# Optimization experiments

Hardware: AMD Instinct MI355X
Metric: run time of the kernel (lower is better)

The kernel has to match this reference:

```python
import jax, jax.numpy as jnp
import numpy as np

# Segment boundaries from the original hard-coded slices: 13,13,13,9,4 repeated twice
SEG_BOUNDS = [0, 13, 26, 39, 48, 52, 65, 78, 91, 100, 104]


def segmented_log_softmax(x):
    # x: [B, 104]; independent log-softmax over each of the 10 fixed segments
    return jnp.concatenate(
        [jax.nn.log_softmax(x[:, a:b], axis=-1)
         for a, b in zip(SEG_BOUNDS[:-1], SEG_BOUNDS[1:])], axis=-1)


def setup_inputs() -> dict:
    key = jax.random.key(0)
    ks = jax.random.split(key, 8)
    B, H, D = 8192, 2048, 104
    return {
        "line": jax.random.normal(ks[0], (B, D), dtype=jnp.float32),
        "hidden": jax.random.normal(ks[1], (B, H), dtype=jnp.float32),
        "U_w": jax.random.normal(ks[2], (H, H), dtype=jnp.float32) * 0.02,
        "U_b": jax.random.normal(ks[3], (H,), dtype=jnp.float32) * 0.02,
        "W_w": jax.random.normal(ks[4], (H, D), dtype=jnp.float32) * 0.02,
        "W_b": jax.random.normal(ks[5], (H,), dtype=jnp.float32) * 0.02,
        "V_w": jax.random.normal(ks[6], (D, H), dtype=jnp.float32) * 0.02,
        "V_b": jax.random.normal(ks[7], (D,), dtype=jnp.float32) * 0.02,
    }


def reference(line, hidden, U_w, U_b, W_w, W_b, V_w, V_b):
    # h_t = sigmoid(U(hidden) + W(line)); torch Linear: y = x @ W.T + b
    h_t = jax.nn.sigmoid(hidden @ U_w.T + U_b + line @ W_w.T + W_b)  # [B, H]
    pred = h_t @ V_w.T + V_b                                          # [B, 104]
    pred_logsoft = segmented_log_softmax(pred)                        # [B, 104]
    return pred_logsoft, h_t
```

## Files before the change

kernel.cpp:

```cpp
#include <hip/hip_runtime.h>
#include <cstdint>
#include <cstddef>


typedef __bf16 bf16x8 __attribute__((ext_vector_type(8)));
typedef float  f32x4  __attribute__((ext_vector_type(4)));
typedef unsigned short ushort8 __attribute__((ext_vector_type(8)));
typedef float  float4v __attribute__((ext_vector_type(4)));

#define BB 8192
#define HH 2048
#define DD 104

static __device__ __forceinline__ unsigned short f2bf(float f) {
  unsigned u = __float_as_uint(f);
  unsigned r = (u + 0x7FFFu + ((u >> 16) & 1u)) >> 16;
  return (unsigned short)r;
}

#define GLD_LDS(g, l)                                                          \
  __builtin_amdgcn_global_load_lds(                                            \
      (__attribute__((address_space(1))) void*)(g),                            \
      (__attribute__((address_space(3))) void*)(l), 16, 0, 0)

#define MEMFENCE asm volatile("" ::: "memory")
#define MFMA16(a, b, c) __builtin_amdgcn_mfma_f32_16x16x32_bf16((a), (b), (c), 0, 0, 0)

__global__ __launch_bounds__(256) void conv_bf16_kernel(
    const float* __restrict__ hidden, const float* __restrict__ Uw,
    unsigned short* __restrict__ out_hidden, unsigned short* __restrict__ out_U) {
  long long i = ((long long)blockIdx.x * blockDim.x + threadIdx.x) * 8;
  const float* src; unsigned short* dst; long long off;
  if (i < (long long)BB * HH) { src = hidden; dst = out_hidden; off = i; }
  else { src = Uw; dst = out_U; off = i - (long long)BB * HH; }
  float4v a = *(const float4v*)(src + off);
  float4v b = *(const float4v*)(src + off + 4);
  ushort8 o;
  o[0]=f2bf(a[0]); o[1]=f2bf(a[1]); o[2]=f2bf(a[2]); o[3]=f2bf(a[3]);
  o[4]=f2bf(b[0]); o[5]=f2bf(b[1]); o[6]=f2bf(b[2]); o[7]=f2bf(b[3]);
  *(ushort8*)(dst + off) = o;
}

__global__ __launch_bounds__(256) void pad_bf16_kernel(
    const float* __restrict__ line, const float* __restrict__ Ww,
    const float* __restrict__ Vw,
    unsigned short* __restrict__ line_pad, unsigned short* __restrict__ Ww_pad,
    unsigned short* __restrict__ Vw_pad) {
  int i = blockIdx.x * blockDim.x + threadIdx.x;
  const int N1 = BB * 128;
  const int N2 = N1 + HH * 128;
  if (i < N1) {
    int r = i >> 7, c = i & 127;
    line_pad[i] = (c < DD) ? f2bf(line[r * DD + c]) : (unsigned short)0;
  } else if (i < N2) {
    int j = i - N1; int r = j >> 7, c = j & 127;
    Ww_pad[j] = (c < DD) ? f2bf(Ww[r * DD + c]) : (unsigned short)0;
  } else {
    int j = i - N2; int r = j >> 11, c = j & 2047;
    Vw_pad[j] = (r < DD) ? f2bf(Vw[r * 2048 + c]) : (unsigned short)0;
  }
}

template <int BUF, bool STAGE, bool TAIL>
static __device__ __forceinline__ void ktile(
    int kb_n,
    unsigned short* smem,
    const unsigned short* pAh, const unsigned short* pAl,
    const unsigned short* pBu, const unsigned short* pBw,
    unsigned short* dA, unsigned short* dB,
    int aoffs, int boffs, f32x4 (&acc)[8][4]) {
  constexpr int SB = BUF ^ 1;
  const unsigned short* Ab = smem + BUF * 16384;
  const unsigned short* Bb = smem + 32768 + BUF * 16384;
  const bool hi = STAGE && (kb_n >= 2048);
  const unsigned short* sA0 = hi ? pAl + (kb_n - 2048) : pAh + kb_n;
  const unsigned short* sB0 = hi ? pBw + (kb_n - 2048) : pBu + kb_n;
  const int rstr = hi ? 128 : 2048;
  bf16x8 a[8], b0, b1;

#pragma unroll
  for (int mi = 0; mi < 8; ++mi) a[mi] = *(const bf16x8*)(Ab + aoffs + mi * 512);
  b0 = *(const bf16x8*)(Bb + boffs);
  b1 = *(const bf16x8*)(Bb + boffs + 512);
  if (STAGE) {
    GLD_LDS(sA0, dA + SB * 16384);
    GLD_LDS(sA0 + 128 * rstr, dA + SB * 16384 + 4096);
  }
  __builtin_amdgcn_s_setprio(1);
#pragma unroll
  for (int mi = 0; mi < 8; ++mi) {
    acc[mi][0] = MFMA16(a[mi], b0, acc[mi][0]);
    acc[mi][1] = MFMA16(a[mi], b1, acc[mi][1]);
  }
  __builtin_amdgcn_s_setprio(0);
  MEMFENCE; __builtin_amdgcn_s_barrier(); MEMFENCE;

  b0 = *(const bf16x8*)(Bb + boffs + 1024);
  b1 = *(const bf16x8*)(Bb + boffs + 1536);
  if (STAGE) {
    GLD_LDS(sB0, dB + SB * 16384);
    GLD_LDS(sB0 + 128 * rstr, dB + SB * 16384 + 4096);
  }
  __builtin_amdgcn_s_setprio(1);
#pragma unroll
  for (int mi = 0; mi < 8; ++mi) {
    acc[mi][2] = MFMA16(a[mi], b0, acc[mi][2]);
    acc[mi][3] = MFMA16(a[mi], b1, acc[mi][3]);
  }
  __builtin_amdgcn_s_setprio(0);
  if (TAIL) { asm volatile("s_waitcnt vmcnt(0)" ::: "memory"); }
  else      { asm volatile("s_waitcnt vmcnt(4)" ::: "memory"); }
  MEMFENCE; __builtin_amdgcn_s_barrier(); MEMFENCE;

#pragma unroll
  for (int mi = 0; mi < 8; ++mi) a[mi] = *(const bf16x8*)(Ab + 8192 + aoffs + mi * 512);
  b0 = *(const bf16x8*)(Bb + 8192 + boffs);
  b1 = *(const bf16x8*)(Bb + 8192 + boffs + 512);
  if (STAGE) {
    GLD_LDS(sA0 + 32, dA + SB * 16384 + 8192);
    GLD_LDS(sA0 + 32 + 128 * rstr, dA + SB * 16384 + 8192 + 4096);
  }
  __builtin_amdgcn_s_setprio(1);
#pragma unroll
  for (int mi = 0; mi < 8; ++mi) {
    acc[mi][0] = MFMA16(a[mi], b0, acc[mi][0]);
    acc[mi][1] = MFMA16(a[mi], b1, acc[mi][1]);
  }
  __builtin_amdgcn_s_setprio(0);
  MEMFENCE; __builtin_amdgcn_s_barrier(); MEMFENCE;

  b0 = *(const bf16x8*)(Bb + 8192 + boffs + 1024);
  b1 = *(const bf16x8*)(Bb + 8192 + boffs + 1536);
  if (STAGE) {
    GLD_LDS(sB0 + 32, dB + SB * 16384 + 8192);
    GLD_LDS(sB0 + 32 + 128 * rstr, dB + SB * 16384 + 8192 + 4096);
  }
  __builtin_amdgcn_s_setprio(1);
#pragma unroll
  for (int mi = 0; mi < 8; ++mi) {
    acc[mi][2] = MFMA16(a[mi], b0, acc[mi][2]);
    acc[mi][3] = MFMA16(a[mi], b1, acc[mi][3]);
  }
  __builtin_amdgcn_s_setprio(0);
  if (!TAIL) { asm volatile("s_waitcnt vmcnt(4)" ::: "memory"); }
  MEMFENCE; __builtin_amdgcn_s_barrier(); MEMFENCE;
}

__global__ __launch_bounds__(512, 2) void gemm1_kernel(
    const unsigned short* __restrict__ Ahid,
    const unsigned short* __restrict__ Aline,
    const unsigned short* __restrict__ BU,
    const unsigned short* __restrict__ BW,
    const float* __restrict__ Ub, const float* __restrict__ Wb,
    float* __restrict__ outH, unsigned short* __restrict__ outHbf) {
  __shared__ unsigned short smem[65536];
  const int t = threadIdx.x;
  const int l = t & 63;
  const int wid = t >> 6;
  const int wr = wid >> 2, wc = wid & 3;

  const int bid = blockIdx.x;
  const int wg = (bid & 7) * 32 + (bid >> 3);
  const int brow = (wg >> 3) * 256;
  const int bcol = (wg & 7) * 256;

  const int frow = l & 15, lhi = l >> 4;
  const int slot8 = (lhi ^ ((frow >> 1) & 3)) * 8;

  const int srow = t >> 2;
  const int scol = (((t & 3) ^ ((t >> 3) & 3)) * 8);
  const unsigned short* pAh = Ahid + (size_t)(brow + srow) * 2048 + scol;
  const unsigned short* pAl = Aline + (size_t)(brow + srow) * 128 + scol;
  const unsigned short* pBu = BU + (size_t)(bcol + srow) * 2048 + scol;
  const unsigned short* pBw = BW + (size_t)(bcol + srow) * 128 + scol;
  unsigned short* dA = smem + t * 8;
  unsigned short* dB = smem + 32768 + t * 8;

  const int aoffs = (wr * 128 + frow) * 32 + slot8;
  const int boffs = (wc * 64 + frow) * 32 + slot8;

  f32x4 acc[8][4] = {};

  GLD_LDS(pAh, dA);
  GLD_LDS(pAh + 128 * 2048, dA + 4096);
  GLD_LDS(pBu, dB);
  GLD_LDS(pBu + 128 * 2048, dB + 4096);
  GLD_LDS(pAh + 32, dA + 8192);
  GLD_LDS(pAh + 32 + 128 * 2048, dA + 8192 + 4096);
  GLD_LDS(pBu + 32, dB + 8192);
  GLD_LDS(pBu + 32 + 128 * 2048, dB + 8192 + 4096);
  asm volatile("s_waitcnt vmcnt(4)" ::: "memory");
  __builtin_amdgcn_s_barrier(); MEMFENCE;

  for (int it = 0; it < 16; ++it) {
    ktile<0, true, false>((2 * it + 1) * 64, smem, pAh, pAl, pBu, pBw, dA, dB, aoffs, boffs, acc);
    ktile<1, true, false>((2 * it + 2) * 64, smem, pAh, pAl, pBu, pBw, dA, dB, aoffs, boffs, acc);
  }
  ktile<0, true, false>(33 * 64, smem, pAh, pAl, pBu, pBw, dA, dB, aoffs, boffs, acc);
  ktile<1, false, true>(0, smem, pAh, pAl, pBu, pBw, dA, dB, aoffs, boffs, acc);

#pragma unroll
  for (int nf = 0; nf < 4; ++nf) {
    const int col = bcol + wc * 64 + nf * 16 + frow;
    const float bias = Ub[col] + Wb[col];
#pragma unroll
    for (int mi = 0; mi < 8; ++mi) {
      const int r0 = brow + wr * 128 + mi * 16 + lhi * 4;
#pragma unroll
      for (int jj = 0; jj < 4; ++jj) {
        const float v = acc[mi][nf][jj] + bias;
        const float h = 1.0f / (1.0f + __expf(-v));
        const size_t idx = (size_t)(r0 + jj) * HH + col;
        outH[idx] = h;
        outHbf[idx] = f2bf(h);
      }
    }
  }
}

template <int NM, int NN>
static __device__ __forceinline__ void mfma_step(
    const unsigned short* sA, const unsigned short* sB, int arow0, int brow0,
    int frow, int fk, f32x4 (&acc)[NM][NN]) {
  bf16x8 af[NM], bfr[NN];
#pragma unroll
  for (int m = 0; m < NM; ++m)
    af[m] = *(const bf16x8*)(sA + (arow0 + m * 16 + frow) * 32 + fk);
#pragma unroll
  for (int n = 0; n < NN; ++n)
    bfr[n] = *(const bf16x8*)(sB + (brow0 + n * 16 + frow) * 32 + fk);
#pragma unroll
  for (int m = 0; m < NM; ++m)
#pragma unroll
    for (int n = 0; n < NN; ++n)
      acc[m][n] = MFMA16(af[m], bfr[n], acc[m][n]);
}

__global__ __launch_bounds__(256, 2) void gemm2_kernel(
    const unsigned short* __restrict__ A,
    const unsigned short* __restrict__ Bm,
    const float* __restrict__ Vb,
    float* __restrict__ outLS) {
  __shared__ unsigned short sA[64 * 32];
  __shared__ unsigned short sB[128 * 32];
  __shared__ float pred[64 * 105];
  const int t = threadIdx.x;
  const int l = t & 63;
  const int wid = t >> 6, wr = wid >> 1, wc = wid & 1;
  const int brow = blockIdx.x * 64;
  const int srow = t >> 2, scg = t & 3;
  const int frow = l & 15, fk = (l >> 4) * 8;

  const unsigned short* gA = A + (size_t)(brow + srow) * HH + scg * 8;
  const unsigned short* gB = Bm + (size_t)srow * HH + scg * 8;
  unsigned short* lA = sA + t * 8;
  unsigned short* lB = sB + t * 8;

  f32x4 acc[2][4] = {};
  for (int ks = 0; ks < 64; ++ks) {
    __syncthreads();
    GLD_LDS(gA, lA);
    GLD_LDS(gB, lB);
    GLD_LDS(gB + 64 * HH, lB + 64 * 32);
    gA += 32; gB += 32;
    __syncthreads();
    mfma_step<2, 4>(sA, sB, wr * 32, wc * 64, frow, fk, acc);
  }

#pragma unroll
  for (int n = 0; n < 4; ++n) {
    const int col = wc * 64 + n * 16 + frow;
    if (col < DD) {
      const float vb = Vb[col];
#pragma unroll
      for (int m = 0; m < 2; ++m) {
        const int r0 = wr * 32 + m * 16 + (l >> 4) * 4;
#pragma unroll
        for (int j = 0; j < 4; ++j)
          pred[(r0 + j) * 105 + col] = acc[m][n][j] + vb;
      }
    }
  }
  __syncthreads();

  if (t < 64) {
    const int segb[11] = {0, 13, 26, 39, 48, 52, 65, 78, 91, 100, 104};
    const float* p = pred + t * 105;
    float* o = outLS + (size_t)(brow + t) * DD;
    for (int s = 0; s < 10; ++s) {
      const int a = segb[s], b = segb[s + 1];
      float mx = -3.0e38f;
      for (int c = a; c < b; ++c) mx = fmaxf(mx, p[c]);
      float sum = 0.0f;
      for (int c = a; c < b; ++c) sum += __expf(p[c] - mx);
      const float ls = __logf(sum) + mx;
      for (int c = a; c < b; ++c) o[c] = p[c] - ls;
    }
  }
}

extern "C" void kernel_launch(void* const* d_in, const int* in_sizes, int n_in,
                              void* d_out, int out_size, void* d_ws, size_t ws_size,
                              hipStream_t stream) {
  (void)in_sizes; (void)n_in; (void)out_size; (void)ws_size;
  const float* line   = (const float*)d_in[0];
  const float* hidden = (const float*)d_in[1];
  const float* Uw     = (const float*)d_in[2];
  const float* Ub     = (const float*)d_in[3];
  const float* Ww     = (const float*)d_in[4];
  const float* Wb     = (const float*)d_in[5];
  const float* Vw     = (const float*)d_in[6];
  const float* Vb     = (const float*)d_in[7];

  char* ws = (char*)d_ws;
  unsigned short* hid_bf  = (unsigned short*)(ws);
  unsigned short* U_bf    = (unsigned short*)(ws + 33554432);
  unsigned short* line_bf = (unsigned short*)(ws + 41943040);
  unsigned short* Ww_bf   = (unsigned short*)(ws + 44040192);
  unsigned short* Vw_bf   = (unsigned short*)(ws + 44564480);
  unsigned short* ht_bf   = (unsigned short*)(ws + 45088768);

  float* outLS = (float*)d_out;
  float* outH  = (float*)d_out + (size_t)BB * DD;

  conv_bf16_kernel<<<10240, 256, 0, stream>>>(hidden, Uw, hid_bf, U_bf);
  pad_bf16_kernel<<<6144, 256, 0, stream>>>(line, Ww, Vw, line_bf, Ww_bf, Vw_bf);
  gemm1_kernel<<<256, 512, 0, stream>>>(hid_bf, line_bf, U_bf, Ww_bf, Ub, Wb,
                                        outH, ht_bf);
  gemm2_kernel<<<128, 256, 0, stream>>>(ht_bf, Vw_bf, Vb, outLS);
}
```

Baseline: 134.9 us.

## Software-pipeline LDS fragment loads with register double-buffering in GEMM1 main loop

Restructures the GEMM1 k-tile loop so the A/B fragments for the next half-tile are read from LDS into a second register set while MFMAs run on the current set. All global-to-LDS loads for the next buffer are issued up front, and barriers drop from four to two per tile. This hides LDS read latency behind MFMA work and cuts synchronisation, at the cost of twice as many fragment registers, which could reduce occupancy at 512 threads with 2 blocks per CU.

```diff
diff --git a/kernel.cpp b/kernel.cpp
--- a/kernel.cpp
+++ b/kernel.cpp
@@ -61,89 +61,72 @@
   }
 }
 
-template <int BUF, bool STAGE, bool TAIL>
-static __device__ __forceinline__ void ktile(
-    int kb_n,
-    unsigned short* smem,
+template <int BUF, bool STAGE>
+static __device__ __forceinline__ void tile_body(
+    int kb_n, unsigned short* smem,
     const unsigned short* pAh, const unsigned short* pAl,
     const unsigned short* pBu, const unsigned short* pBw,
     unsigned short* dA, unsigned short* dB,
-    int aoffs, int boffs, f32x4 (&acc)[8][4]) {
+    int aoffs, int boffs,
+    bf16x8 (&ac)[8], bf16x8 (&bc)[4], bf16x8 (&an)[8], bf16x8 (&bn)[4],
+    f32x4 (&acc)[8][4]) {
   constexpr int SB = BUF ^ 1;
-  const unsigned short* Ab = smem + BUF * 16384;
-  const unsigned short* Bb = smem + 32768 + BUF * 16384;
-  const bool hi = STAGE && (kb_n >= 2048);
-  const unsigned short* sA0 = hi ? pAl + (kb_n - 2048) : pAh + kb_n;
-  const unsigned short* sB0 = hi ? pBw + (kb_n - 2048) : pBu + kb_n;
-  const int rstr = hi ? 128 : 2048;
-  bf16x8 a[8], b0, b1;
-
-#pragma unroll
-  for (int mi = 0; mi < 8; ++mi) a[mi] = *(const bf16x8*)(Ab + aoffs + mi * 512);
-  b0 = *(const bf16x8*)(Bb + boffs);
-  b1 = *(const bf16x8*)(Bb + boffs + 512);
-  if (STAGE) {
+  const unsigned short* Ab  = smem + BUF * 16384;
+  const unsigned short* Bb  = smem + 32768 + BUF * 16384;
+  const unsigned short* Ab2 = smem + SB * 16384;
+  const unsigned short* Bb2 = smem + 32768 + SB * 16384;
+
+  if constexpr (STAGE) {
+    const bool hi = (kb_n >= 2048);
+    const unsigned short* sA0 = hi ? pAl + (kb_n - 2048) : pAh + kb_n;
+    const unsigned short* sB0 = hi ? pBw + (kb_n - 2048) : pBu + kb_n;
+    const int rstr = hi ? 128 : 2048;
     GLD_LDS(sA0, dA + SB * 16384);
     GLD_LDS(sA0 + 128 * rstr, dA + SB * 16384 + 4096);
-  }
-  __builtin_amdgcn_s_setprio(1);
-#pragma unroll
-  for (int mi = 0; mi < 8; ++mi) {
-    acc[mi][0] = MFMA16(a[mi], b0, acc[mi][0]);
-    acc[mi][1] = MFMA16(a[mi], b1, acc[mi][1]);
-  }
-  __builtin_amdgcn_s_setprio(0);
-  MEMFENCE; __builtin_amdgcn_s_barrier(); MEMFENCE;
-
-  b0 = *(const bf16x8*)(Bb + boffs + 1024);
-  b1 = *(const bf16x8*)(Bb + boffs + 1536);
-  if (STAGE) {
     GLD_LDS(sB0, dB + SB * 16384);
     GLD_LDS(sB0 + 128 * rstr, dB + SB * 16384 + 4096);
-  }
-  __builtin_amdgcn_s_setprio(1);
-#pragma unroll
-  for (int mi = 0; mi < 8; ++mi) {
-    acc[mi][2] = MFMA16(a[mi], b0, acc[mi][2]);
-    acc[mi][3] = MFMA16(a[mi], b1, acc[mi][3]);
-  }
-  __builtin_amdgcn_s_setprio(0);
-  if (TAIL) { asm volatile("s_waitcnt vmcnt(0)" ::: "memory"); }
-  else      { asm volatile("s_waitcnt vmcnt(4)" ::: "memory"); }
-  MEMFENCE; __builtin_amdgcn_s_barrier(); MEMFENCE;
-
-#pragma unroll
-  for (int mi = 0; mi < 8; ++mi) a[mi] = *(const bf16x8*)(Ab + 8192 + aoffs + mi * 512);
-  b0 = *(const bf16x8*)(Bb + 8192 + boffs);
-  b1 = *(const bf16x8*)(Bb + 8192 + boffs + 512);
-  if (STAGE) {
     GLD_LDS(sA0 + 32, dA + SB * 16384 + 8192);
     GLD_LDS(sA0 + 32 + 128 * rstr, dA + SB * 16384 + 8192 + 4096);
-  }
-  __builtin_amdgcn_s_setprio(1);
-#pragma unroll
-  for (int mi = 0; mi < 8; ++mi) {
-    acc[mi][0] = MFMA16(a[mi], b0, acc[mi][0]);
-    acc[mi][1] = MFMA16(a[mi], b1, acc[mi][1]);
-  }
-  __builtin_amdgcn_s_setprio(0);
-  MEMFENCE; __builtin_amdgcn_s_barrier(); MEMFENCE;
-
-  b0 = *(const bf16x8*)(Bb + 8192 + boffs + 1024);
-  b1 = *(const bf16x8*)(Bb + 8192 + boffs + 1536);
-  if (STAGE) {
     GLD_LDS(sB0 + 32, dB + SB * 16384 + 8192);
     GLD_LDS(sB0 + 32 + 128 * rstr, dB + SB * 16384 + 8192 + 4096);
-  }
+    asm volatile("s_waitcnt vmcnt(8)" ::: "memory");
+  } else {
+    asm volatile("s_waitcnt vmcnt(0)" ::: "memory");
+  }
+  MEMFENCE; __builtin_amdgcn_s_barrier(); MEMFENCE;
+#pragma unroll
+  for (int mi = 0; mi < 8; ++mi)
+    an[mi] = *(const bf16x8*)(Ab + 8192 + aoffs + mi * 512);
+#pragma unroll
+  for (int nf = 0; nf < 4; ++nf)
+    bn[nf] = *(const bf16x8*)(Bb + 8192 + boffs + nf * 512);
   __builtin_amdgcn_s_setprio(1);
 #pragma unroll
-  for (int mi = 0; mi < 8; ++mi) {
-    acc[mi][2] = MFMA16(a[mi], b0, acc[mi][2]);
-    acc[mi][3] = MFMA16(a[mi], b1, acc[mi][3]);
-  }
+  for (int mi = 0; mi < 8; ++mi)
+#pragma unroll
+    for (int nf = 0; nf < 4; ++nf)
+      acc[mi][nf] = MFMA16(ac[mi], bc[nf], acc[mi][nf]);
   __builtin_amdgcn_s_setprio(0);
-  if (!TAIL) { asm volatile("s_waitcnt vmcnt(4)" ::: "memory"); }
+
+  if constexpr (STAGE) {
+    asm volatile("s_waitcnt vmcnt(4)" ::: "memory");
+  }
   MEMFENCE; __builtin_amdgcn_s_barrier(); MEMFENCE;
+  if constexpr (STAGE) {
+#pragma unroll
+    for (int mi = 0; mi < 8; ++mi)
+      ac[mi] = *(const bf16x8*)(Ab2 + aoffs + mi * 512);
+#pragma unroll
+    for (int nf = 0; nf < 4; ++nf)
+      bc[nf] = *(const bf16x8*)(Bb2 + boffs + nf * 512);
+  }
+  __builtin_amdgcn_s_setprio(1);
+#pragma unroll
+  for (int mi = 0; mi < 8; ++mi)
+#pragma unroll
+    for (int nf = 0; nf < 4; ++nf)
+      acc[mi][nf] = MFMA16(an[mi], bn[nf], acc[mi][nf]);
+  __builtin_amdgcn_s_setprio(0);
 }
 
 __global__ __launch_bounds__(512, 2) void gemm1_kernel(
@@ -189,15 +172,27 @@
   GLD_LDS(pAh + 32 + 128 * 2048, dA + 8192 + 4096);
   GLD_LDS(pBu + 32, dB + 8192);
   GLD_LDS(pBu + 32 + 128 * 2048, dB + 8192 + 4096);
-  asm volatile("s_waitcnt vmcnt(4)" ::: "memory");
-  __builtin_amdgcn_s_barrier(); MEMFENCE;
+  asm volatile("s_waitcnt vmcnt(0)" ::: "memory");
+  MEMFENCE; __builtin_amdgcn_s_barrier(); MEMFENCE;
+
+  bf16x8 ac[8], bc[4], an[8], bn[4];
+#pragma unroll
+  for (int mi = 0; mi < 8; ++mi)
+    ac[mi] = *(const bf16x8*)(smem + aoffs + mi * 512);
+#pragma unroll
+  for (int nf = 0; nf < 4; ++nf)
+    bc[nf] = *(const bf16x8*)(smem + 32768 + boffs + nf * 512);
 
   for (int it = 0; it < 16; ++it) {
-    ktile<0, true, false>((2 * it + 1) * 64, smem, pAh, pAl, pBu, pBw, dA, dB, aoffs, boffs, acc);
-    ktile<1, true, false>((2 * it + 2) * 64, smem, pAh, pAl, pBu, pBw, dA, dB, aoffs, boffs, acc);
-  }
-  ktile<0, true, false>(33 * 64, smem, pAh, pAl, pBu, pBw, dA, dB, aoffs, boffs, acc);
-  ktile<1, false, true>(0, smem, pAh, pAl, pBu, pBw, dA, dB, aoffs, boffs, acc);
+    tile_body<0, true>((2 * it + 1) * 64, smem, pAh, pAl, pBu, pBw, dA, dB,
+                       aoffs, boffs, ac, bc, an, bn, acc);
+    tile_body<1, true>((2 * it + 2) * 64, smem, pAh, pAl, pBu, pBw, dA, dB,
+                       aoffs, boffs, ac, bc, an, bn, acc);
+  }
+  tile_body<0, true>(33 * 64, smem, pAh, pAl, pBu, pBw, dA, dB,
+                     aoffs, boffs, ac, bc, an, bn, acc);
+  tile_body<1, false>(0, smem, pAh, pAl, pBu, pBw, dA, dB,
+                      aoffs, boffs, ac, bc, an, bn, acc);
 
 #pragma unroll
   for (int nf = 0; nf < 4; ++nf) {
```

New measurement: 146.7 us. +8.8%, slower.
